# Kernel optimization log

Measured on AMD Instinct MI355X. Metric: run time of the kernel, lower is better.

## Reference

```python
import jax, jax.numpy as jnp
import numpy as np
import jax.scipy.linalg as jsl
from jax import lax

N_SAMPLES = 16384
N_COMPONENTS = 16
N_FEATURES = 128
EPS = 1e-3
MAX_DEPTH = 8
JITTER = 1e-6
LOG_2PI = float(np.log(2.0 * np.pi))


def _em_update(x, means, covs):
    # One call of update_parameters(): weights are (un-normalized) mahalanobis
    # distances computed with the OLD means/covariances; diffs for the
    # covariance update also use the OLD means (diff is computed before the
    # in-place mean assignment in the torch code).
    d = x.shape[1]
    inv = jnp.linalg.inv(covs)                      # [K,D,D]
    diff = x[:, None, :] - means[None, :, :]        # [N,K,D]
    sol = jnp.einsum('kde,nke->nkd', inv, diff)     # [N,K,D]
    w = jnp.einsum('nkd,nkd->nk', diff, sol)        # [N,K] mahalanobis dists
    sw = w.sum(axis=0)                              # [K]
    new_means = jnp.einsum('nk,nd->kd', w, x) / sw[:, None]
    outer = jnp.einsum('nk,nkd,nke->kde', w, diff, diff)
    new_covs = outer / sw[:, None, None] + JITTER * jnp.eye(d, dtype=x.dtype)
    return new_means, new_covs


def _em_loop(x, means, covs):
    # Faithful to the torch while-loop: update first, then check convergence
    # of the means (Frobenius norm) against eps, up to max_depth iterations.
    def cond(c):
        _, _, _, depth, done = c
        return jnp.logical_and(depth < MAX_DEPTH, jnp.logical_not(done))

    def body(c):
        m, cv, prev, depth, _ = c
        nm, nc = _em_update(x, m, cv)
        diff = jnp.linalg.norm(nm - prev)
        done = diff <= EPS
        return (nm, nc, nm, depth + 1, done)

    init = (means, covs, means, jnp.int32(0), jnp.bool_(False))
    m, cv, _, _, _ = lax.while_loop(cond, body, init)
    return m, cv


def _log_prob(x, means, covs):
    # MultivariateNormal.log_prob for each component, batched over K via
    # Cholesky (matching torch.distributions internals).
    d = x.shape[1]
    L = jnp.linalg.cholesky(covs)                   # [K,D,D]
    diff = x[:, None, :] - means[None, :, :]        # [N,K,D]
    # per-component triangular solve: L_k y = diff[:,k,:]^T -> y [K,D,N]
    y = jax.vmap(lambda Lk, dk: jsl.solve_triangular(Lk, dk.T, lower=True),
                 in_axes=(0, 1))(L, diff)
    maha = jnp.sum(y * y, axis=1)                   # [K,N]
    logdet = 2.0 * jnp.sum(jnp.log(jnp.diagonal(L, axis1=-2, axis2=-1)), axis=-1)  # [K]
    return -0.5 * (d * LOG_2PI + logdet[:, None] + maha)  # [K,N]


def _forward(x, means, covariances, weights):
    # torch.no_grad() EM loop -> stop_gradient on loop inputs/outputs
    m0 = lax.stop_gradient(means)
    c0 = lax.stop_gradient(covariances)
    xs = lax.stop_gradient(x)
    m_loop, c_loop = _em_loop(xs, m0, c0)
    # final update_parameters call (training path, outside no_grad)
    m_fin, c_fin = _em_update(x, m_loop, c_loop)
    logp = _log_prob(x, m_fin, c_fin)               # [K,N]
    loss = -jnp.sum(weights[:, None] * logp)
    return loss, m_fin, c_fin


def setup_inputs() -> dict:
    key = jax.random.key(0)
    k1, k2 = jax.random.split(key)
    x = jax.random.normal(k1, (N_SAMPLES, N_FEATURES), dtype=jnp.float32)
    means = jax.random.normal(k2, (N_COMPONENTS, N_FEATURES), dtype=jnp.float32)
    covariances = jnp.tile(jnp.eye(N_FEATURES, dtype=jnp.float32),
                           (N_COMPONENTS, 1, 1))
    weights = jnp.ones((N_COMPONENTS,), jnp.float32) / N_COMPONENTS
    return {"x": x, "means": means, "covariances": covariances,
            "weights": weights}


def reference(x, means, covariances, weights):
    return _forward(x, means, covariances, weights)
```

## Files before the change

kernel.cpp:

```cpp
#include <hip/hip_runtime.h>
#include <math.h>


#define NS 16384
#define DD 128
#define KC 16
#define JITTER_ 1e-6f
#define EPS2_ 1e-6f
#define LOG_2PI_ 1.8378770664093454f
#define NCHUNK 1024

typedef __attribute__((ext_vector_type(8))) short bf16x8;
typedef __attribute__((ext_vector_type(16))) float f32x16;

enum : int {
  OFF_CUR_M  = 0,
  OFF_CS     = 2048,
  OFF_T      = 528384,
  OFF_LOGDET = 530432,
  OFF_SW     = 530448,
  OFF_NUM    = 530464,
  OFF_W      = 532512,
  OFF_LOSSK  = 794656,
  OFF_DIFFSQ = 794672,
  OFF_DONE   = 794673,
  OFF_CTR    = 794674,
  OFF_XAH    = 794676,
  OFF_XAL    = 1843252,
  OFF_XBH    = 2891828,
  OFF_XBL    = 3940404,
  OFF_LBH    = 4988980,
  OFF_LBL    = 5120052,
  WS_FLOATS  = 5251124
};

__device__ __forceinline__ float bf2f(ushort u) {
  union { unsigned u; float f; } c; c.u = ((unsigned)u) << 16; return c.f;
}
__device__ __forceinline__ ushort f2bf_rne(float f) {
  union { float f; unsigned u; } c; c.f = f;
  unsigned r = c.u + 0x7fffu + ((c.u >> 16) & 1u);
  return (ushort)(r >> 16);
}
__device__ __forceinline__ ushort f2bf_trunc(float f) {
  union { float f; unsigned u; } c; c.f = f; return (ushort)(c.u >> 16);
}

__device__ __forceinline__ int swz(int r, int c) {
  return (r << 7) + ((((c >> 2) + r) & 31) << 2) + (c & 3);
}

__device__ __forceinline__ float rdlane(float v, int lane) {
  union { float f; int i; } c; c.f = v;
  c.i = __builtin_amdgcn_readlane(c.i, lane);
  return c.f;
}

__device__ __forceinline__ void frag_write(const float* Zs, ushort* LBH,
                                           ushort* LBL, int g) {
  int ll = g & 63, ks2 = (g >> 6) & 1, ec = (g >> 7) & 3, dg = (g >> 9) & 3;
  int d = 32 * dg + (ll & 31);
  int e = 32 * ec + 16 * ks2 + 8 * (ll >> 5);
  float4 z0 = *(const float4*)&Zs[d * 132 + e];
  float4 z1 = *(const float4*)&Zs[d * 132 + e + 4];
  float zv[8] = {z0.x, z0.y, z0.z, z0.w, z1.x, z1.y, z1.z, z1.w};
  ushort hh[8], lo2[8];
  #pragma unroll
  for (int j = 0; j < 8; ++j) {
    hh[j]  = f2bf_trunc(zv[j]);
    lo2[j] = f2bf_rne(zv[j] - bf2f(hh[j]));
  }
  *(ushort4*)&LBH[g * 8]     = make_ushort4(hh[0], hh[1], hh[2], hh[3]);
  *(ushort4*)&LBH[g * 8 + 4] = make_ushort4(hh[4], hh[5], hh[6], hh[7]);
  *(ushort4*)&LBL[g * 8]     = make_ushort4(lo2[0], lo2[1], lo2[2], lo2[3]);
  *(ushort4*)&LBL[g * 8 + 4] = make_ushort4(lo2[4], lo2[5], lo2[6], lo2[7]);
}

__global__ __launch_bounds__(256) void k_init_split(const float* __restrict__ x,
                                                    const float* __restrict__ means,
                                                    const float* __restrict__ covs,
                                                    float* __restrict__ ws) {
  __shared__ float xt[64 * 132];
  int b = blockIdx.x, t = threadIdx.x;
  int idx = b * 256 + t;
  for (int i = idx; i < KC * DD * DD; i += 256 * 256) ws[OFF_CS + i] = covs[i];
  if (idx < KC * DD) ws[OFF_CUR_M + idx] = means[idx];
  if (idx == 0) {
    ws[OFF_DIFFSQ] = 0.f;
    ((int*)ws)[OFF_DONE] = 0;
    ((int*)ws)[OFF_CTR]  = 0;
  }
  int n0 = b * 64;
  for (int fi = t; fi < 2048; fi += 256) {
    int n = fi >> 5, q = (fi & 31) * 4;
    *(float4*)&xt[n * 132 + q] = *(const float4*)&x[(size_t)(n0 + n) * DD + q];
  }
  __syncthreads();
  ushort* __restrict__ XAH = (ushort*)(ws + OFF_XAH);
  ushort* __restrict__ XAL = (ushort*)(ws + OFF_XAL);
  ushort* __restrict__ XBH = (ushort*)(ws + OFF_XBH);
  ushort* __restrict__ XBL = (ushort*)(ws + OFF_XBL);
  for (int s = t; s < 1024; s += 256) {
    int l = s & 63, ks = (s >> 6) & 1, ec = (s >> 7) & 3, ngl = (s >> 9) & 1;
    int nl = 32 * ngl + (l & 31);
    int e0 = 32 * ec + 16 * ks + 8 * (l >> 5);
    float vv[8];
    *(float4*)&vv[0] = *(const float4*)&xt[nl * 132 + e0];
    *(float4*)&vv[4] = *(const float4*)&xt[nl * 132 + e0 + 4];
    ushort h[8], lo[8];
    #pragma unroll
    for (int j = 0; j < 8; ++j) {
      h[j]  = f2bf_trunc(vv[j]);
      lo[j] = f2bf_rne(vv[j] - bf2f(h[j]));
    }
    size_t base = ((((size_t)((n0 >> 5) + ngl) * 4 + ec) * 2 + ks) * 64 + l) * 8;
    *(ushort4*)&XAH[base]     = make_ushort4(h[0], h[1], h[2], h[3]);
    *(ushort4*)&XAH[base + 4] = make_ushort4(h[4], h[5], h[6], h[7]);
    *(ushort4*)&XAL[base]     = make_ushort4(lo[0], lo[1], lo[2], lo[3]);
    *(ushort4*)&XAL[base + 4] = make_ushort4(lo[4], lo[5], lo[6], lo[7]);
  }
  for (int s = t; s < 1024; s += 256) {
    int l = s & 63, nbl = (s >> 6) & 3, eg = (s >> 8) & 3;
    int e = 32 * eg + (l & 31);
    int nl = 16 * nbl + 8 * (l >> 5);
    ushort h[8], lo[8];
    #pragma unroll
    for (int j = 0; j < 8; ++j) {
      float v = xt[(nl + j) * 132 + e];
      h[j]  = f2bf_trunc(v);
      lo[j] = f2bf_rne(v - bf2f(h[j]));
    }
    size_t base = (((size_t)eg * (NS / 16) + (n0 >> 4) + nbl) * 64 + l) * 8;
    *(ushort4*)&XBH[base]     = make_ushort4(h[0], h[1], h[2], h[3]);
    *(ushort4*)&XBH[base + 4] = make_ushort4(h[4], h[5], h[6], h[7]);
    *(ushort4*)&XBL[base]     = make_ushort4(lo[0], lo[1], lo[2], lo[3]);
    *(ushort4*)&XBL[base + 4] = make_ushort4(lo[4], lo[5], lo[6], lo[7]);
  }
}

__global__ __launch_bounds__(512) void k_fused(float* __restrict__ ws, float* __restrict__ dout,
                                               int guarded, int do_update, int write_out,
                                               int accum_diff, int final_pass) {
  if (guarded && ((const int*)ws)[OFF_DONE]) return;
  __shared__ float m[DD * DD];
  __shared__ float Zs[DD * 132];
  __shared__ float Ws[64 * 68];
  __shared__ float invd_s[DD];
  __shared__ float cm_s[DD], nm_s[DD];
  __shared__ float redbuf[2];
  int k = blockIdx.x, t = threadIdx.x;
  int l = t & 63, wv = t >> 6;
  float* __restrict__ CS = ws + OFF_CS + (size_t)k * DD * DD;

  if (do_update) {
    float sw = ws[OFF_SW + k];
    float inv = 1.f / sw;
    float4 s4v[8];
    #pragma unroll
    for (int it = 0; it < 8; ++it)
      s4v[it] = *(const float4*)&CS[(it * 512 + t) * 4];
    if (t < DD) {
      cm_s[t] = ws[OFF_CUR_M + k * DD + t];
      nm_s[t] = ws[OFF_NUM + k * DD + t];
    }
    __syncthreads();
    float* __restrict__ doutC = dout + 1 + KC * DD + (size_t)k * DD * DD;
    #pragma unroll
    for (int it = 0; it < 8; ++it) {
      int idx = (it * 512 + t) * 4;
      float4 s4 = s4v[it];
      int d = idx >> 7, e = idx & 127;
      float md = cm_s[d], nd = nm_s[d];
      float4 me4 = *(const float4*)&cm_s[e];
      float4 ne4 = *(const float4*)&nm_s[e];
      float4 v;
      v.x = (s4.x - md * ne4.x - nd * me4.x + sw * md * me4.x) * inv;
      v.y = (s4.y - md * ne4.y - nd * me4.y + sw * md * me4.y) * inv;
      v.z = (s4.z - md * ne4.z - nd * me4.z + sw * md * me4.z) * inv;
      v.w = (s4.w - md * ne4.w - nd * me4.w + sw * md * me4.w) * inv;
      if (d >= e && d < e + 4) (&v.x)[d - e] += JITTER_;
      *(float4*)&m[swz(d, e)] = v;
      if (write_out) *(float4*)&doutC[idx] = v;
    }
    if (t < DD) {
      float me = cm_s[t], ne = nm_s[t];
      float newm = ne * inv;
      ws[OFF_CUR_M + k * DD + t] = newm;
      if (write_out) dout[1 + k * DD + t] = newm;
      if (accum_diff) {
        float dm = newm - me;
        float s = dm * dm;
        #pragma unroll
        for (int mk2 = 1; mk2 < 64; mk2 <<= 1) s += __shfl_xor(s, mk2, 64);
        if (l == 0) redbuf[wv] = s;
      }
      ws[OFF_NUM + k * DD + t] = 0.f;
    }
    if (t == 0) {
      ws[OFF_SW + k] = 0.f;
      if (final_pass) ws[OFF_LOSSK + k] = 0.f;
    }
  } else {
    #pragma unroll
    for (int it = 0; it < 8; ++it) {
      int idx = (it * 512 + t) * 4;
      float4 c4 = *(const float4*)&CS[idx];
      *(float4*)&m[swz(idx >> 7, idx & 127)] = c4;
    }
    if (t < DD) ws[OFF_NUM + k * DD + t] = 0.f;
    if (t == 0) ws[OFF_SW + k] = 0.f;
  }
  __syncthreads();

  auto FACTOR = [&](int P) {
    int ra = P + l, rb = P + 64 + l;
    bool isA = (wv == 0);
    bool va = ra < DD, vb = rb < DD;
    float A[16], B[16];
    if (va) {
      #pragma unroll
      for (int q = 0; q < 4; ++q) {
        float4 v = *(const float4*)&m[swz(ra, P + 4 * q)];
        A[4*q+0] = v.x; A[4*q+1] = v.y; A[4*q+2] = v.z; A[4*q+3] = v.w;
      }
    }
    if (!isA && vb) {
      #pragma unroll
      for (int q = 0; q < 4; ++q) {
        float4 v = *(const float4*)&m[swz(rb, P + 4 * q)];
        B[4*q+0] = v.x; B[4*q+1] = v.y; B[4*q+2] = v.z; B[4*q+3] = v.w;
      }
    }
    #pragma unroll
    for (int jj = 0; jj < 16; ++jj) {
      float dj = rdlane(A[jj], jj);
      float inv = __builtin_amdgcn_rsqf(dj);
      inv = inv * (1.5f - 0.5f * dj * inv * inv);
      float sj = dj * inv;
      if (va) {
        if (l == jj) A[jj] = sj;
        else if (l > jj) A[jj] *= inv;
      }
      if (!isA && vb) B[jj] *= inv;
      #pragma unroll
      for (int jj2 = jj + 1; jj2 < 16; ++jj2) {
        float c = rdlane(A[jj], jj2);
        if (va && l > jj) A[jj2] -= A[jj] * c;
        if (!isA && vb) B[jj2] -= B[jj] * c;
      }
    }
    if (isA && va) {
      #pragma unroll
      for (int q = 0; q < 4; ++q)
        *(float4*)&m[swz(ra, P + 4 * q)] = make_float4(A[4*q], A[4*q+1], A[4*q+2], A[4*q+3]);
    }
    if (!isA && vb) {
      #pragma unroll
      for (int q = 0; q < 4; ++q)
        *(float4*)&m[swz(rb, P + 4 * q)] = make_float4(B[4*q], B[4*q+1], B[4*q+2], B[4*q+3]);
    }
  };
  auto TILE8 = [&](int i0, int q0, int P) {
    float acc8[8][8] = {};
    #pragma unroll
    for (int pq = 0; pq < 4; ++pq) {
      float4 a[8], b[8];
      #pragma unroll
      for (int r = 0; r < 8; ++r) a[r] = *(const float4*)&m[swz(i0 + r, P + 4 * pq)];
      #pragma unroll
      for (int c = 0; c < 8; ++c) b[c] = *(const float4*)&m[swz(q0 + c, P + 4 * pq)];
      #pragma unroll
      for (int r = 0; r < 8; ++r)
        #pragma unroll
        for (int c = 0; c < 8; ++c)
          acc8[r][c] += a[r].x * b[c].x + a[r].y * b[c].y +
                        a[r].z * b[c].z + a[r].w * b[c].w;
    }
    #pragma unroll
    for (int r = 0; r < 8; ++r)
      #pragma unroll
      for (int cq = 0; cq < 2; ++cq) {
        float4 v = *(const float4*)&m[swz(i0 + r, q0 + 4 * cq)];
        v.x -= acc8[r][4*cq+0]; v.y -= acc8[r][4*cq+1];
        v.z -= acc8[r][4*cq+2]; v.w -= acc8[r][4*cq+3];
        *(float4*)&m[swz(i0 + r, q0 + 4 * cq)] = v;
      }
  };

  if (wv < 2) FACTOR(0);
  __syncthreads();
  for (int P = 0; P < DD - 16; P += 16) {
    int C0 = P + 16;
    int nts = ((DD - C0) >> 1) * 4;
    for (int idx = t; idx < nts; idx += 512) {
      int r0 = C0 + 2 * (idx >> 2), q0 = C0 + 4 * (idx & 3);
      float acc2[2][4] = {};
      #pragma unroll
      for (int pq = 0; pq < 4; ++pq) {
        float4 a0 = *(const float4*)&m[swz(r0, P + 4 * pq)];
        float4 a1 = *(const float4*)&m[swz(r0 + 1, P + 4 * pq)];
        float4 b[4];
        #pragma unroll
        for (int c = 0; c < 4; ++c) b[c] = *(const float4*)&m[swz(q0 + c, P + 4 * pq)];
        #pragma unroll
        for (int c = 0; c < 4; ++c) {
          acc2[0][c] += a0.x * b[c].x + a0.y * b[c].y + a0.z * b[c].z + a0.w * b[c].w;
          acc2[1][c] += a1.x * b[c].x + a1.y * b[c].y + a1.z * b[c].z + a1.w * b[c].w;
        }
      }
      float4 v0 = *(const float4*)&m[swz(r0, q0)];
      v0.x -= acc2[0][0]; v0.y -= acc2[0][1]; v0.z -= acc2[0][2]; v0.w -= acc2[0][3];
      *(float4*)&m[swz(r0, q0)] = v0;
      float4 v1 = *(const float4*)&m[swz(r0 + 1, q0)];
      v1.x -= acc2[1][0]; v1.y -= acc2[1][1]; v1.z -= acc2[1][2]; v1.w -= acc2[1][3];
      *(float4*)&m[swz(r0 + 1, q0)] = v1;
    }
    __syncthreads();
    if (wv < 2) {
      FACTOR(C0);
    } else {
      int R0 = P + 32, s = DD - R0;
      if (s > 0) {
        int nt = s >> 3, tri = (nt * (nt + 1)) >> 1;
        for (int idx = t - 128; idx < tri; idx += 384) {
          int ti = (int)(0.5f * (sqrtf(8.f * (float)idx + 1.f) - 1.f));
          while (((ti + 1) * (ti + 2)) >> 1 <= idx) ++ti;
          while ((ti * (ti + 1)) >> 1 > idx) --ti;
          int tj = idx - ((ti * (ti + 1)) >> 1);
          TILE8(R0 + 8 * ti, R0 + 8 * tj, P);
        }
      }
    }
    __syncthreads();
  }

  if (t < DD) {
    float dv = m[swz(t, t)];
    invd_s[t] = 1.f / dv;
    if (final_pass) {
      float lg = logf(dv);
      #pragma unroll
      for (int mk2 = 1; mk2 < 64; mk2 <<= 1) lg += __shfl_xor(lg, mk2, 64);
      if (l == 0) redbuf[wv] = lg;
    }
  }
  __syncthreads();
  if (wv < 4) {
    int j = l & 31, r0 = 32 * wv, row = r0 + (l & 31);
    float M[32];
    #pragma unroll
    for (int q = 0; q < 8; ++q) {
      float4 v = *(const float4*)&m[swz(row, r0 + 4 * q)];
      M[4*q+0] = v.x; M[4*q+1] = v.y; M[4*q+2] = v.z; M[4*q+3] = v.w;
    }
    float acc[32];
    #pragma unroll
    for (int i2 = 0; i2 < 32; ++i2) acc[i2] = 0.f;
    #pragma unroll
    for (int p = 0; p < 32; ++p) {
      float zp = (((p == j) ? 1.f : 0.f) - acc[p]) * invd_s[r0 + p];
      Zs[(r0 + p) * 132 + r0 + j] = zp;
      #pragma unroll
      for (int i2 = p + 1; i2 < 32; ++i2)
        acc[i2] += rdlane(M[p], i2) * zp;
    }
  } else {
    for (int z = t - 256; z < 1536; z += 256) {
      int r, c;
      if (z < 1024) { r = z >> 4; c = 64 + ((z & 15) << 2); }
      else { int z2 = z - 1024; int h = z2 >> 8; int z3 = z2 & 255;
             r = h * 64 + (z3 >> 3); c = h * 64 + 32 + ((z3 & 7) << 2); }
      *(float4*)&Zs[r * 132 + c] = make_float4(0.f, 0.f, 0.f, 0.f);
    }
    if (final_pass && t == 256) ws[OFF_LOGDET + k] = 2.f * (redbuf[0] + redbuf[1]);
  }
  __syncthreads();
  {
    int h = t >> 8, i = (t >> 3) & 31, j0 = (t & 7) << 2;
    int rI = h * 64 + 32 + i, cb = h * 64;
    float ax = 0.f, ay = 0.f, az = 0.f, aw = 0.f;
    #pragma unroll
    for (int q0 = 0; q0 < 32; q0 += 4) {
      float4 a  = *(const float4*)&m[swz(rI, cb + q0)];
      float4 z0 = *(const float4*)&Zs[(cb + q0 + 0) * 132 + cb + j0];
      float4 z1 = *(const float4*)&Zs[(cb + q0 + 1) * 132 + cb + j0];
      float4 z2 = *(const float4*)&Zs[(cb + q0 + 2) * 132 + cb + j0];
      float4 z3 = *(const float4*)&Zs[(cb + q0 + 3) * 132 + cb + j0];
      ax += a.x * z0.x + a.y * z1.x + a.z * z2.x + a.w * z3.x;
      ay += a.x * z0.y + a.y * z1.y + a.z * z2.y + a.w * z3.y;
      az += a.x * z0.z + a.y * z1.z + a.z * z2.z + a.w * z3.z;
      aw += a.x * z0.w + a.y * z1.w + a.z * z2.w + a.w * z3.w;
    }
    *(float4*)&Ws[(h * 32 + i) * 68 + j0] = make_float4(ax, ay, az, aw);
  }
  __syncthreads();
  {
    int h = t >> 8, i = (t >> 3) & 31, j0 = (t & 7) << 2;
    int rI = h * 64 + 32 + i;
    float ax = 0.f, ay = 0.f, az = 0.f, aw = 0.f;
    #pragma unroll
    for (int q0 = 0; q0 < 32; q0 += 4) {
      float4 a  = *(const float4*)&Zs[rI * 132 + h * 64 + 32 + q0];
      float4 w0 = *(const float4*)&Ws[(h * 32 + q0 + 0) * 68 + j0];
      float4 w1 = *(const float4*)&Ws[(h * 32 + q0 + 1) * 68 + j0];
      float4 w2 = *(const float4*)&Ws[(h * 32 + q0 + 2) * 68 + j0];
      float4 w3 = *(const float4*)&Ws[(h * 32 + q0 + 3) * 68 + j0];
      ax += a.x * w0.x + a.y * w1.x + a.z * w2.x + a.w * w3.x;
      ay += a.x * w0.y + a.y * w1.y + a.z * w2.y + a.w * w3.y;
      az += a.x * w0.z + a.y * w1.z + a.z * w2.z + a.w * w3.z;
      aw += a.x * w0.w + a.y * w1.w + a.z * w2.w + a.w * w3.w;
    }
    *(float4*)&Zs[rI * 132 + h * 64 + j0] = make_float4(-ax, -ay, -az, -aw);
  }
  __syncthreads();
  ushort* __restrict__ LBH = (ushort*)(ws + OFF_LBH) + (size_t)k * 16384;
  ushort* __restrict__ LBL = (ushort*)(ws + OFF_LBL) + (size_t)k * 16384;
  if (t < 128) {
    int i0 = (t >> 4) << 3, j0 = (t & 15) << 2;
    float acc4[8][4] = {};
    for (int q0 = 0; q0 < 64; q0 += 4) {
      float4 a[8], b[4];
      #pragma unroll
      for (int r = 0; r < 8; ++r) a[r] = *(const float4*)&m[swz(64 + i0 + r, q0)];
      #pragma unroll
      for (int s2 = 0; s2 < 4; ++s2) b[s2] = *(const float4*)&Zs[(q0 + s2) * 132 + j0];
      #pragma unroll
      for (int r = 0; r < 8; ++r) {
        acc4[r][0] += a[r].x * b[0].x + a[r].y * b[1].x + a[r].z * b[2].x + a[r].w * b[3].x;
        acc4[r][1] += a[r].x * b[0].y + a[r].y * b[1].y + a[r].z * b[2].y + a[r].w * b[3].y;
        acc4[r][2] += a[r].x * b[0].z + a[r].y * b[1].z + a[r].z * b[2].z + a[r].w * b[3].z;
        acc4[r][3] += a[r].x * b[0].w + a[r].y * b[1].w + a[r].z * b[2].w + a[r].w * b[3].w;
      }
    }
    #pragma unroll
    for (int r = 0; r < 8; ++r)
      *(float4*)&Ws[(i0 + r) * 68 + j0] =
          make_float4(acc4[r][0], acc4[r][1], acc4[r][2], acc4[r][3]);
  } else {
    #pragma unroll
    for (int it = 0; it < 2; ++it) frag_write(Zs, LBH, LBL, (t - 128) + it * 384);
  }
  __syncthreads();
  if (t < 128) {
    int i0 = (t >> 4) << 3, j0 = (t & 15) << 2;
    float acc4[8][4] = {};
    for (int q0 = 0; q0 < 64; q0 += 4) {
      float4 a[8], b[4];
      #pragma unroll
      for (int r = 0; r < 8; ++r)
        a[r] = *(const float4*)&Zs[(64 + i0 + r) * 132 + 64 + q0];
      #pragma unroll
      for (int s2 = 0; s2 < 4; ++s2) b[s2] = *(const float4*)&Ws[(q0 + s2) * 68 + j0];
      #pragma unroll
      for (int r = 0; r < 8; ++r) {
        acc4[r][0] += a[r].x * b[0].x + a[r].y * b[1].x + a[r].z * b[2].x + a[r].w * b[3].x;
        acc4[r][1] += a[r].x * b[0].y + a[r].y * b[1].y + a[r].z * b[2].y + a[r].w * b[3].y;
        acc4[r][2] += a[r].x * b[0].z + a[r].y * b[1].z + a[r].z * b[2].z + a[r].w * b[3].z;
        acc4[r][3] += a[r].x * b[0].w + a[r].y * b[1].w + a[r].z * b[2].w + a[r].w * b[3].w;
      }
    }
    #pragma unroll
    for (int r = 0; r < 8; ++r)
      *(float4*)&Zs[(64 + i0 + r) * 132 + j0] =
          make_float4(-acc4[r][0], -acc4[r][1], -acc4[r][2], -acc4[r][3]);
  } else {
    #pragma unroll
    for (int it = 0; it < 2; ++it) {
      int r = 768 + (t - 128) + it * 384;
      int g;
      if (r < 1024) g = r;
      else { int rr = r - 1024;
             g = (2 + (rr >> 8)) * 512 + (2 + ((rr >> 7) & 1)) * 128 + (rr & 127); }
      frag_write(Zs, LBH, LBL, g);
    }
  }
  __syncthreads();
  if (t < DD) {
    const float* __restrict__ mk = ws + OFF_CUR_M + k * DD;
    float s0 = 0.f;
    for (int e = 0; e < DD; e += 4) {
      float4 z = *(const float4*)&Zs[t * 132 + e];
      s0 += z.x * mk[e] + z.y * mk[e + 1] + z.z * mk[e + 2] + z.w * mk[e + 3];
    }
    ws[OFF_T + k * DD + t] = s0;
  } else {
    for (int rr = t - 128; rr < 512; rr += 384) {
      int g = (2 + (rr >> 8)) * 512 + ((rr >> 7) & 1) * 128 + (rr & 127);
      frag_write(Zs, LBH, LBL, g);
    }
  }
  if (accum_diff && t == 0) {
    atomicAdd(&ws[OFF_DIFFSQ], redbuf[0] + redbuf[1]);
    __threadfence();
    int old = atomicAdd((int*)ws + OFF_CTR, 1);
    if ((old & (KC - 1)) == KC - 1) {
      float v = atomicAdd(&ws[OFF_DIFFSQ], 0.f);
      if (v <= EPS2_) atomicExch((int*)ws + OFF_DONE, 1);
      atomicExch(&ws[OFF_DIFFSQ], 0.f);
    }
  }
}

__global__ __launch_bounds__(256) void k_quad(float* __restrict__ ws,
                                              const float* __restrict__ wts,
                                              int guarded, int final_pass) {
  if (guarded && ((const int*)ws)[OFF_DONE]) return;
  __shared__ float warr[128];
  int k = blockIdx.y, bx = blockIdx.x, t = threadIdx.x;
  int l = t & 63, wv = t >> 6;
  int n0 = bx * 128;
  if (t < 128) ws[OFF_CS + (size_t)k * DD * DD + bx * 128 + t] = 0.f;
  const ushort* __restrict__ XAH = (const ushort*)(ws + OFF_XAH);
  const ushort* __restrict__ XAL = (const ushort*)(ws + OFF_XAL);
  const ushort* __restrict__ LBH = (const ushort*)(ws + OFF_LBH) + (size_t)k * 16384;
  const ushort* __restrict__ LBL = (const ushort*)(ws + OFF_LBL) + (size_t)k * 16384;
  f32x16 acc[4] = {};
  size_t ng4 = (size_t)(4 * bx + wv) * 4;
  #pragma unroll
  for (int ec = 0; ec < 4; ++ec) {
    #pragma unroll
    for (int ks = 0; ks < 2; ++ks) {
      size_t aoff = (((ng4 + ec) * 2 + ks) * 64 + l) * 8;
      bf16x8 ah = *(const bf16x8*)&XAH[aoff];
      bf16x8 al = *(const bf16x8*)&XAL[aoff];
      #pragma unroll
      for (int dg = 0; dg < 4; ++dg) {
        size_t boff = ((((size_t)dg * 4 + ec) * 2 + ks) * 64 + l) * 8;
        bf16x8 bh = *(const bf16x8*)&LBH[boff];
        bf16x8 bl = *(const bf16x8*)&LBL[boff];
        acc[dg] = __builtin_amdgcn_mfma_f32_32x32x16_bf16(ah, bh, acc[dg], 0, 0, 0);
        acc[dg] = __builtin_amdgcn_mfma_f32_32x32x16_bf16(ah, bl, acc[dg], 0, 0, 0);
        acc[dg] = __builtin_amdgcn_mfma_f32_32x32x16_bf16(al, bh, acc[dg], 0, 0, 0);
      }
    }
  }
  float tv[4];
  #pragma unroll
  for (int c = 0; c < 4; ++c) tv[c] = ws[OFF_T + k * DD + 32 * c + (l & 31)];
  float part[16];
  #pragma unroll
  for (int r = 0; r < 16; ++r) {
    float s = 0.f;
    #pragma unroll
    for (int c = 0; c < 4; ++c) { float d = acc[c][r] - tv[c]; s += d * d; }
    part[r] = s;
  }
  #pragma unroll
  for (int mk2 = 1; mk2 < 32; mk2 <<= 1)
    #pragma unroll
    for (int r = 0; r < 16; ++r) part[r] += __shfl_xor(part[r], mk2, 64);
  int h = l >> 5;
  if ((l & 31) < 16) {
    int r = l & 31;
    int row = (r & 3) + 8 * (r >> 2) + 4 * h + 32 * wv;
    ws[OFF_W + k * NS + n0 + row] = part[r];
    if (final_pass) warr[row] = part[r];
  }
  if (final_pass) {
    __syncthreads();
    if (t < 64) {
      float s = warr[t] + warr[t + 64];
      #pragma unroll
      for (int mk2 = 1; mk2 < 64; mk2 <<= 1) s += __shfl_xor(s, mk2, 64);
      if (t == 0) atomicAdd(&ws[OFF_LOSSK + k], 0.5f * wts[k] * s);
    }
  }
}

__global__ __launch_bounds__(256, 2) void k_scatter(float* __restrict__ ws, int guarded) {
  if (guarded && ((const int*)ws)[OFF_DONE]) return;
  __shared__ float Sred[8192];
  int id = blockIdx.x, t = threadIdx.x;
  int xcd = id & 7, j = id >> 3;
  int chunk = xcd + 8 * (j & 1);
  int dg = (j >> 1) & 3;
  int k = j >> 3;
  int l = t & 63, wv = t >> 6;
  const ushort* __restrict__ XBH = (const ushort*)(ws + OFF_XBH);
  const ushort* __restrict__ XBL = (const ushort*)(ws + OFF_XBL);
  const float* __restrict__ wp = ws + OFF_W + k * NS + chunk * NCHUNK;
  f32x16 acc[4] = {};
  int nb0 = chunk * (NCHUNK / 16) + wv * (NCHUNK / 64);
  int ko = (l >> 5) * 8;
  float zsum = 0.f, wsum = 0.f;
  size_t aoff = (((size_t)dg * (NS / 16) + nb0) * 64 + l) * 8;
  bf16x8 th = *(const bf16x8*)&XBH[aoff];
  bf16x8 tl = *(const bf16x8*)&XBL[aoff];
  float4 w0 = *(const float4*)&wp[16 * (wv * (NCHUNK / 64)) + ko];
  float4 w1 = *(const float4*)&wp[16 * (wv * (NCHUNK / 64)) + ko + 4];
  for (int st = 0; st < NCHUNK / 64; ++st) {
    bf16x8 bh[4], bl[4];
    #pragma unroll
    for (int eg = 0; eg < 4; ++eg) {
      size_t boff = (((size_t)eg * (NS / 16) + nb0 + st) * 64 + l) * 8;
      bh[eg] = *(const bf16x8*)&XBH[boff];
      bl[eg] = *(const bf16x8*)&XBL[boff];
    }
    int stn = (st + 1) & (NCHUNK / 64 - 1);
    size_t aoffn = (((size_t)dg * (NS / 16) + nb0 + stn) * 64 + l) * 8;
    bf16x8 thn = *(const bf16x8*)&XBH[aoffn];
    bf16x8 tln = *(const bf16x8*)&XBL[aoffn];
    int wbn = 16 * (wv * (NCHUNK / 64) + stn) + ko;
    float4 w0n = *(const float4*)&wp[wbn];
    float4 w1n = *(const float4*)&wp[wbn + 4];
    float wj[8] = {w0.x, w0.y, w0.z, w0.w, w1.x, w1.y, w1.z, w1.w};
    bf16x8 ah, al;
    #pragma unroll
    for (int jj = 0; jj < 8; ++jj) {
      float xf = bf2f((ushort)th[jj]) + bf2f((ushort)tl[jj]);
      float zf = wj[jj] * xf;
      zsum += zf;
      union { float f; unsigned u; } cz; cz.f = zf;
      ah[jj] = (short)(ushort)(cz.u >> 16);
      union { unsigned u; float f; } ch; ch.u = cz.u & 0xffff0000u;
      al[jj] = (short)f2bf_rne(zf - ch.f);
    }
    if (dg == 0 && (l & 31) == 0) {
      #pragma unroll
      for (int jj = 0; jj < 8; ++jj) wsum += wj[jj];
    }
    #pragma unroll
    for (int eg = 0; eg < 4; ++eg) {
      acc[eg] = __builtin_amdgcn_mfma_f32_32x32x16_bf16(ah, bh[eg], acc[eg], 0, 0, 0);
      acc[eg] = __builtin_amdgcn_mfma_f32_32x32x16_bf16(ah, bl[eg], acc[eg], 0, 0, 0);
      acc[eg] = __builtin_amdgcn_mfma_f32_32x32x16_bf16(al, bh[eg], acc[eg], 0, 0, 0);
    }
    th = thn; tl = tln; w0 = w0n; w1 = w1n;
  }
  zsum += __shfl_xor(zsum, 32, 64);
  if (l < 32) atomicAdd(&ws[OFF_NUM + k * DD + 32 * dg + l], zsum);
  if (dg == 0) {
    wsum += __shfl_xor(wsum, 32, 64);
    if (l == 0) atomicAdd(&ws[OFF_SW + k], wsum);
  }
  float* __restrict__ S = ws + OFF_CS + (size_t)k * DD * DD;
  #pragma unroll
  for (int p = 0; p < 2; ++p) {
    if (p) __syncthreads();
    #pragma unroll
    for (int egL = 0; egL < 2; ++egL)
      #pragma unroll
      for (int r = 0; r < 16; ++r)
        Sred[(wv * 2 + egL) * 1024 + r * 64 + l] = acc[2 * p + egL][r];
    __syncthreads();
    #pragma unroll
    for (int i = 0; i < 8; ++i) {
      int idx = i * 256 + t;
      int ll = idx & 63, r = (idx >> 6) & 15, egL = idx >> 10;
      int base = egL * 1024 + r * 64 + ll;
      float s = Sred[base] + Sred[base + 2048] + Sred[base + 4096] + Sred[base + 6144];
      int h = ll >> 5;
      int drow = 32 * dg + (r & 3) + 8 * (r >> 2) + 4 * h;
      int e = 32 * (2 * p + egL) + (ll & 31);
      atomicAdd(&S[drow * DD + e], s);
    }
  }
}

__global__ void k_lossfin(const float* __restrict__ weights, const float* __restrict__ ws,
                          float* __restrict__ dout) {
  if (threadIdx.x == 0 && blockIdx.x == 0) {
    float base = 0.f;
    for (int k = 0; k < KC; ++k)
      base += weights[k] * 0.5f * (float)NS * ((float)DD * LOG_2PI_ + ws[OFF_LOGDET + k])
            + ws[OFF_LOSSK + k];
    dout[0] = base;
  }
}

extern "C" void kernel_launch(void* const* d_in, const int* in_sizes, int n_in,
                              void* d_out, int out_size, void* d_ws, size_t ws_size,
                              hipStream_t stream) {
  const float* x       = (const float*)d_in[0];
  const float* means   = (const float*)d_in[1];
  const float* covs    = (const float*)d_in[2];
  const float* weights = (const float*)d_in[3];
  float* out = (float*)d_out;
  float* ws  = (float*)d_ws;

  hipLaunchKernelGGL(k_init_split, dim3(NS / 64), dim3(256), 0, stream, x, means, covs, ws);
  hipLaunchKernelGGL(k_fused, dim3(16), dim3(512), 0, stream, ws, out, 0, 0, 0, 0, 0);

  for (int u = 0; u < 8; ++u) {
    hipLaunchKernelGGL(k_quad,    dim3(128, 16), dim3(256), 0, stream, ws, weights, 1, 0);
    hipLaunchKernelGGL(k_scatter, dim3(1024), dim3(256), 0, stream, ws, 1);
    hipLaunchKernelGGL(k_fused,   dim3(16), dim3(512), 0, stream, ws, out, 1, 1, 0, 1, 0);
  }

  hipLaunchKernelGGL(k_quad,    dim3(128, 16), dim3(256), 0, stream, ws, weights, 0, 0);
  hipLaunchKernelGGL(k_scatter, dim3(1024), dim3(256), 0, stream, ws, 0);
  hipLaunchKernelGGL(k_fused,   dim3(16), dim3(512), 0, stream, ws, out, 0, 1, 1, 0, 1);
  hipLaunchKernelGGL(k_quad,    dim3(128, 16), dim3(256), 0, stream, ws, weights, 0, 1);
  hipLaunchKernelGGL(k_lossfin, dim3(1), dim3(64), 0, stream, weights, ws, out);
}
```

Measured before the change: 812.0 us.

## Fold panel trailing update into factor step to remove a block barrier

Drops the separate block-wide pass that applied the previous panel's rank-16 update to the next panel columns, along with the __syncthreads after it. The factoring waves now apply that correction themselves from registers using cross-lane reads before factoring. This cuts one barrier per panel step in the blocked Cholesky and lets the other waves start their trailing tile updates earlier. In exchange the two factoring waves do more serial work, with many extra rdlane shuffles, on the critical path.

Result: slower. 832.9 us (+2.6%).

```diff
diff --git a/kernel.cpp b/kernel.cpp
--- a/kernel.cpp
+++ b/kernel.cpp
@@ -212,7 +212,7 @@
   }
   __syncthreads();
 
-  auto FACTOR = [&](int P) {
+  auto FACTOR = [&](int P, int P0, bool corr) {
     int ra = P + l, rb = P + 64 + l;
     bool isA = (wv == 0);
     bool va = ra < DD, vb = rb < DD;
@@ -229,6 +229,46 @@
       for (int q = 0; q < 4; ++q) {
         float4 v = *(const float4*)&m[swz(rb, P + 4 * q)];
         B[4*q+0] = v.x; B[4*q+1] = v.y; B[4*q+2] = v.z; B[4*q+3] = v.w;
+      }
+    }
+    if (corr) {
+      if (isA) {
+        float4 rp[4];
+        if (va) {
+          #pragma unroll
+          for (int q = 0; q < 4; ++q) rp[q] = *(const float4*)&m[swz(ra, P0 + 4 * q)];
+        }
+        #pragma unroll
+        for (int jj = 0; jj < 16; ++jj) {
+          float acc = 0.f;
+          #pragma unroll
+          for (int pq = 0; pq < 4; ++pq) {
+            float bx = rdlane(rp[pq].x, jj), by = rdlane(rp[pq].y, jj);
+            float bz = rdlane(rp[pq].z, jj), bw = rdlane(rp[pq].w, jj);
+            acc += rp[pq].x * bx + rp[pq].y * by + rp[pq].z * bz + rp[pq].w * bw;
+          }
+          if (va) A[jj] -= acc;
+        }
+      } else {
+        float4 bp[4], cp[4];
+        int rc = P + l; if (rc > DD - 1) rc = DD - 1;
+        #pragma unroll
+        for (int q = 0; q < 4; ++q) cp[q] = *(const float4*)&m[swz(rc, P0 + 4 * q)];
+        if (vb) {
+          #pragma unroll
+          for (int q = 0; q < 4; ++q) bp[q] = *(const float4*)&m[swz(rb, P0 + 4 * q)];
+        }
+        #pragma unroll
+        for (int jj = 0; jj < 16; ++jj) {
+          float acc = 0.f;
+          #pragma unroll
+          for (int pq = 0; pq < 4; ++pq) {
+            float bx = rdlane(cp[pq].x, jj), by = rdlane(cp[pq].y, jj);
+            float bz = rdlane(cp[pq].z, jj), bw = rdlane(cp[pq].w, jj);
+            acc += bp[pq].x * bx + bp[pq].y * by + bp[pq].z * bz + bp[pq].w * bw;
+          }
+          if (vb) B[jj] -= acc;
+        }
       }
     }
     #pragma unroll
@@ -287,37 +327,12 @@
       }
   };
 
-  if (wv < 2) FACTOR(0);
+  if (wv < 2) FACTOR(0, 0, false);
   __syncthreads();
   for (int P = 0; P < DD - 16; P += 16) {
     int C0 = P + 16;
-    int nts = ((DD - C0) >> 1) * 4;
-    for (int idx = t; idx < nts; idx += 512) {
-      int r0 = C0 + 2 * (idx >> 2), q0 = C0 + 4 * (idx & 3);
-      float acc2[2][4] = {};
-      #pragma unroll
-      for (int pq = 0; pq < 4; ++pq) {
-        float4 a0 = *(const float4*)&m[swz(r0, P + 4 * pq)];
-        float4 a1 = *(const float4*)&m[swz(r0 + 1, P + 4 * pq)];
-        float4 b[4];
-        #pragma unroll
-        for (int c = 0; c < 4; ++c) b[c] = *(const float4*)&m[swz(q0 + c, P + 4 * pq)];
-        #pragma unroll
-        for (int c = 0; c < 4; ++c) {
-          acc2[0][c] += a0.x * b[c].x + a0.y * b[c].y + a0.z * b[c].z + a0.w * b[c].w;
-          acc2[1][c] += a1.x * b[c].x + a1.y * b[c].y + a1.z * b[c].z + a1.w * b[c].w;
-        }
-      }
-      float4 v0 = *(const float4*)&m[swz(r0, q0)];
-      v0.x -= acc2[0][0]; v0.y -= acc2[0][1]; v0.z -= acc2[0][2]; v0.w -= acc2[0][3];
-      *(float4*)&m[swz(r0, q0)] = v0;
-      float4 v1 = *(const float4*)&m[swz(r0 + 1, q0)];
-      v1.x -= acc2[1][0]; v1.y -= acc2[1][1]; v1.z -= acc2[1][2]; v1.w -= acc2[1][3];
-      *(float4*)&m[swz(r0 + 1, q0)] = v1;
-    }
-    __syncthreads();
     if (wv < 2) {
-      FACTOR(C0);
+      FACTOR(C0, P, true);
     } else {
       int R0 = P + 32, s = DD - R0;
       if (s > 0) {
```
